# Kernel optimization log

Hardware: AMD Instinct MI355X
Metric: run time of the kernel (lower is better)

## Reference

```python
import jax, jax.numpy as jnp
import numpy as np

MARGIN = 1.0
N, D = 8192, 128
NUM_CLASSES = 1024


def setup_inputs() -> dict:
    key = jax.random.key(0)
    k1, k2, k3 = jax.random.split(key, 3)
    a = jax.random.normal(k1, (N, D), dtype=jnp.float32)
    b = jax.random.normal(k2, (N, D), dtype=jnp.float32)
    # L2-normalize embeddings (standard for metric learning; keeps exp() stable)
    a = a / jnp.linalg.norm(a, axis=1, keepdims=True)
    b = b / jnp.linalg.norm(b, axis=1, keepdims=True)
    labels = jax.random.randint(k3, (N,), 0, NUM_CLASSES, dtype=jnp.int64 if jax.config.jax_enable_x64 else jnp.int32)
    return {"a": a, "b": b, "labels": labels}


def reference(a, b, labels):
    # S[i, j] = a_i . b_j  -- full pairwise similarity, one GEMM
    S = a @ b.T  # [N, N]
    same = labels[:, None] == labels[None, :]  # [N, N]
    eye = jnp.eye(labels.shape[0], dtype=bool)
    pos_mask = same & ~eye          # ordered positive pairs (i != j, same label)
    neg_mask = ~same                # ordered negative pairs (labels differ)
    # V[i] = sum_k in neg(i) exp(margin + S[i, k])
    V = jnp.sum(jnp.where(neg_mask, jnp.exp(MARGIN + S), 0.0), axis=1)  # [N]
    # per positive pair (i, j): max(log(V_i + V_j) - S_ij, 0)^2
    hinge = jnp.maximum(jnp.log(V[:, None] + V[None, :]) - S, 0.0)
    comp = jnp.where(pos_mask, hinge * hinge, 0.0)
    num_pos = jnp.sum(pos_mask)
    loss = jnp.sum(comp) / (2.0 * num_pos.astype(S.dtype))
    return loss
```

## Files before the change

kernel.cpp:

```cpp
#include <hip/hip_runtime.h>

#define NN 8192
#define DD 128
#define MAXCLS 64
#define NCHUNK 8
#define LOG2E 1.4426950408889634f
#define E1    2.718281828459045f

typedef __attribute__((ext_vector_type(8))) short bf16x8;
typedef __attribute__((ext_vector_type(4))) float f32x4;

#if __has_builtin(__builtin_amdgcn_exp2f)
#define EXP2F(x) __builtin_amdgcn_exp2f(x)
#else
#define EXP2F(x) exp2f(x)
#endif

__device__ __forceinline__ void load16_lds(const unsigned short* g, unsigned short* l) {
    __builtin_amdgcn_global_load_lds(
        (const __attribute__((address_space(1))) unsigned int*)g,
        (__attribute__((address_space(3))) unsigned int*)l,
        16, 0, 0);
}

__device__ __forceinline__ unsigned short f2bf(float x) {
    unsigned u = __float_as_uint(x);
    u = (u + 0x7FFFu + ((u >> 16) & 1u)) >> 16;
    return (unsigned short)u;
}

__global__ __launch_bounds__(256) void ml_convert_kernel(
    const float* __restrict__ a, const float* __restrict__ b,
    const int* __restrict__ labels,
    unsigned short* __restrict__ abf, unsigned short* __restrict__ bbf,
    int* __restrict__ cnt, int* __restrict__ list)
{
    int t = blockIdx.x * 256 + threadIdx.x;
    const float* src = a;
    unsigned short* dst = abf;
    int idx = t;
    float scale = LOG2E;
    if (t >= 262144) { src = b; dst = bbf; idx = t - 262144; scale = 1.0f; }
    float4 v = ((const float4*)src)[idx];
    ushort4 o;
    o.x = f2bf(v.x * scale); o.y = f2bf(v.y * scale);
    o.z = f2bf(v.z * scale); o.w = f2bf(v.w * scale);
    ((ushort4*)dst)[idx] = o;

    if (t < NN) {
        int c = labels[t];
        int p = atomicAdd(&cnt[c], 1);
        if (p < MAXCLS) list[c * MAXCLS + p] = t;
    }
}

__global__ __launch_bounds__(256, 2) void ml_vsum_gemm_kernel(
    const unsigned short* __restrict__ abf, const unsigned short* __restrict__ bbf,
    float* __restrict__ Vp)
{
    __shared__ unsigned short As[128 * DD];
    __shared__ unsigned short Bs[2][64 * DD];
    __shared__ float red[2][64];

    const int tid  = threadIdx.x;
    const int lane = tid & 63;
    const int wv   = tid >> 6;
    const int row0 = blockIdx.y * 128;
    const int j0   = blockIdx.x * 1024;

    const int lr = lane >> 4;
    const int sp = lane & 15;
    const int m  = lane & 15;
    const int q  = lane >> 4;
    const int xr = m & 7;

#pragma unroll
    for (int i = 0; i < 8; i++) {
        int rb = wv * 32 + i * 4;
        int r  = rb + lr;
        int cc = sp ^ (r & 7);
        load16_lds(&abf[(size_t)(row0 + r) * DD + cc * 8], &As[rb * DD]);
    }
#pragma unroll
    for (int i = 0; i < 4; i++) {
        int rb = wv * 16 + i * 4;
        int r  = rb + lr;
        int cc = sp ^ (r & 7);
        load16_lds(&bbf[(size_t)(j0 + r) * DD + cc * 8], &Bs[0][rb * DD]);
    }
#pragma unroll
    for (int i = 0; i < 4; i++) {
        int rb = wv * 16 + i * 4;
        int r  = rb + lr;
        int cc = sp ^ (r & 7);
        load16_lds(&bbf[(size_t)(j0 + 64 + r) * DD + cc * 8], &Bs[1][rb * DD]);
    }
    __syncthreads();

    const int wi = (wv >> 1) * 64;
    const int wj = (wv & 1) * 32;

    bf16x8 afr[4][4];
#pragma unroll
    for (int ti = 0; ti < 4; ti++)
#pragma unroll
        for (int ks = 0; ks < 4; ks++) {
            int r   = wi + ti * 16 + m;
            int pos = (ks * 4 + q) ^ xr;
            afr[ti][ks] = *(const bf16x8*)(&As[r * DD + pos * 8]);
        }

    float rs[4][4];
#pragma unroll
    for (int ti = 0; ti < 4; ti++)
#pragma unroll
        for (int rg = 0; rg < 4; rg++) rs[ti][rg] = 0.f;

    const f32x4 zero = {0.f, 0.f, 0.f, 0.f};

#pragma unroll 2
    for (int jt = 0; jt < 16; jt++) {
        const int pb = jt & 1;
        f32x4 acc[4][2];
#pragma unroll
        for (int ti = 0; ti < 4; ti++)
#pragma unroll
            for (int tj = 0; tj < 2; tj++) acc[ti][tj] = zero;

#pragma unroll
        for (int ks = 0; ks < 4; ks++) {
            bf16x8 bfr[2];
#pragma unroll
            for (int tj = 0; tj < 2; tj++) {
                int r   = wj + tj * 16 + m;
                int pos = (ks * 4 + q) ^ xr;
                bfr[tj] = *(const bf16x8*)(&Bs[pb][r * DD + pos * 8]);
            }
#pragma unroll
            for (int ti = 0; ti < 4; ti++)
#pragma unroll
                for (int tj = 0; tj < 2; tj++)
                    acc[ti][tj] = __builtin_amdgcn_mfma_f32_16x16x32_bf16(afr[ti][ks], bfr[tj], acc[ti][tj], 0, 0, 0);
        }

#pragma unroll
        for (int ti = 0; ti < 4; ti++)
#pragma unroll
            for (int tj = 0; tj < 2; tj++) {
                f32x4 c = acc[ti][tj];
                rs[ti][0] += EXP2F(c[0]);
                rs[ti][1] += EXP2F(c[1]);
                rs[ti][2] += EXP2F(c[2]);
                rs[ti][3] += EXP2F(c[3]);
            }

        __syncthreads();
        if (jt < 14) {
            int jb = j0 + (jt + 2) * 64;
#pragma unroll
            for (int i = 0; i < 4; i++) {
                int rb = wv * 16 + i * 4;
                int r  = rb + lr;
                int cc = sp ^ (r & 7);
                load16_lds(&bbf[(size_t)(jb + r) * DD + cc * 8], &Bs[pb][rb * DD]);
            }
        }
    }

#pragma unroll
    for (int ti = 0; ti < 4; ti++)
#pragma unroll
        for (int rg = 0; rg < 4; rg++) {
            float v = rs[ti][rg];
            v += __shfl_xor(v, 1);
            v += __shfl_xor(v, 2);
            v += __shfl_xor(v, 4);
            v += __shfl_xor(v, 8);
            rs[ti][rg] = v;
        }

    if ((wv & 1) == 1 && m == 0) {
#pragma unroll
        for (int ti = 0; ti < 4; ti++)
#pragma unroll
            for (int rg = 0; rg < 4; rg++)
                red[wv >> 1][ti * 16 + q * 4 + rg] = rs[ti][rg];
    }
    __syncthreads();
    if ((wv & 1) == 0 && m == 0) {
#pragma unroll
        for (int ti = 0; ti < 4; ti++)
#pragma unroll
            for (int rg = 0; rg < 4; rg++) {
                int rloc = ti * 16 + q * 4 + rg;
                Vp[(size_t)blockIdx.x * NN + row0 + wi + rloc] = rs[ti][rg] + red[wv >> 1][rloc];
            }
    }
}

__global__ __launch_bounds__(256) void ml_pairs_kernel(
    const float* __restrict__ a, const float* __restrict__ b,
    const int* __restrict__ cnt, const int* __restrict__ list,
    const float* __restrict__ Vp,
    float* __restrict__ classLoss, int* __restrict__ classCnt)
{
    __shared__ int   mem[MAXCLS];
    __shared__ float sumExp[MAXCLS];
    __shared__ float Vadj[MAXCLS];
    __shared__ float Sc[MAXCLS * MAXCLS];
    __shared__ float ps[4];
    __shared__ int   cs[4];

    const int c   = blockIdx.x;
    const int tid = threadIdx.x;
    int mc = cnt[c];
    if (mc > MAXCLS) mc = MAXCLS;

    float vsum = 0.f;
    if (tid < mc) {
        int r = list[c * MAXCLS + tid];
        mem[tid] = r;
#pragma unroll
        for (int jc = 0; jc < NCHUNK; jc++) vsum += Vp[(size_t)jc * NN + r];
    }
    if (tid < MAXCLS) sumExp[tid] = 0.f;
    __syncthreads();

    const int g = tid >> 4;
    const int l = tid & 15;
    const int tot1 = mc * mc;
    for (int pp = g; pp < tot1; pp += 16) {
        int i = pp / mc;
        int j = pp - i * mc;
        int ri = mem[i], rj = mem[j];
        const float4* ar = (const float4*)(a + (size_t)ri * DD) + l * 2;
        const float4* br = (const float4*)(b + (size_t)rj * DD) + l * 2;
        float4 a0 = ar[0], a1 = ar[1];
        float4 b0 = br[0], b1 = br[1];
        float s = 0.f;
        s = fmaf(a0.x, b0.x, s); s = fmaf(a0.y, b0.y, s);
        s = fmaf(a0.z, b0.z, s); s = fmaf(a0.w, b0.w, s);
        s = fmaf(a1.x, b1.x, s); s = fmaf(a1.y, b1.y, s);
        s = fmaf(a1.z, b1.z, s); s = fmaf(a1.w, b1.w, s);
        s += __shfl_xor(s, 1);
        s += __shfl_xor(s, 2);
        s += __shfl_xor(s, 4);
        s += __shfl_xor(s, 8);
        if (l == 0) {
            Sc[i * MAXCLS + j] = s;
            atomicAdd(&sumExp[i], __expf(s));
        }
    }
    __syncthreads();

    if (tid < mc) Vadj[tid] = E1 * (vsum - sumExp[tid]);
    __syncthreads();

    float partial = 0.f;
    int   count   = 0;
    for (int pp = tid; pp < tot1; pp += 256) {
        int i = pp / mc;
        int j = pp - i * mc;
        if (i != j) {
            float h = fmaxf(logf(Vadj[i] + Vadj[j]) - Sc[i * MAXCLS + j], 0.f);
            partial += h * h;
            count++;
        }
    }
    for (int off = 32; off > 0; off >>= 1) {
        partial += __shfl_down(partial, off);
        count   += __shfl_down(count, off);
    }
    const int lane = tid & 63, wv = tid >> 6;
    if (lane == 0) { ps[wv] = partial; cs[wv] = count; }
    __syncthreads();
    if (tid == 0) {
        classLoss[c] = ps[0] + ps[1] + ps[2] + ps[3];
        classCnt[c]  = cs[0] + cs[1] + cs[2] + cs[3];
    }
}

__global__ __launch_bounds__(256) void ml_finalize_kernel(
    const float* __restrict__ classLoss, const int* __restrict__ classCnt,
    float* __restrict__ out)
{
    __shared__ double dred[4];
    __shared__ long long cred[4];
    const int tid = threadIdx.x;
    const int lane = tid & 63, wv = tid >> 6;

    double dls = 0.0;
    long long dct = 0;
    for (int k = tid; k < 1024; k += 256) {
        dls += (double)classLoss[k];
        dct += (long long)classCnt[k];
    }
    for (int off = 32; off > 0; off >>= 1) {
        dls += __shfl_down(dls, off);
        dct += __shfl_down(dct, off);
    }
    if (lane == 0) { dred[wv] = dls; cred[wv] = dct; }
    __syncthreads();
    if (tid == 0) {
        double ls = dred[0] + dred[1] + dred[2] + dred[3];
        long long np = cred[0] + cred[1] + cred[2] + cred[3];
        out[0] = (float)(ls / (2.0 * (double)np));
    }
}

extern "C" void kernel_launch(void* const* d_in, const int* in_sizes, int n_in,
                              void* d_out, int out_size, void* d_ws, size_t ws_size,
                              hipStream_t stream)
{
    const float* a      = (const float*)d_in[0];
    const float* b      = (const float*)d_in[1];
    const int*   labels = (const int*)d_in[2];
    float* out = (float*)d_out;

    char* ws = (char*)d_ws;
    unsigned short* abf = (unsigned short*)ws;
    unsigned short* bbf = (unsigned short*)(ws + 2097152);
    char*     base2     = ws + 4194304;
    int*      cnt       = (int*)(base2);
    float*    classLoss = (float*)(base2 + 8192);
    int*      classCnt  = (int*)(base2 + 12288);
    int*      list      = (int*)(base2 + 16384);
    float*    Vp        = (float*)(base2 + 278528);

    (void)hipMemsetAsync(cnt, 0, 4096, stream);

    ml_convert_kernel<<<2048, 256, 0, stream>>>(a, b, labels, abf, bbf, cnt, list);

    dim3 g(NCHUNK, NN / 128);
    ml_vsum_gemm_kernel<<<g, 256, 0, stream>>>(abf, bbf, Vp);

    ml_pairs_kernel<<<1024, 256, 0, stream>>>(a, b, cnt, list, Vp, classLoss, classCnt);

    ml_finalize_kernel<<<1, 256, 0, stream>>>(classLoss, classCnt, out);
}
```

Measured before the change: 104.7 us.

## Split GEMM column range finer, drop A LDS staging, bin labels in pairs kernel

The V-sum GEMM now splits the column range into 16 chunks instead of 8, doubling the grid. Each wave owns 32 rows by 64 columns, with its A fragments loaded straight from global memory instead of staged through LDS. The cross-wave LDS reduction is removed, and launch bounds are raised to allow 4 blocks per CU. Label binning moves out of the convert kernel: each class block scans all labels itself, which removes the memset and the global atomics. The costs are more partial V sums for the pairs kernel to combine and a redundant label scan in every class block.

New measurement: 118.1 us. 1.13x slower.

```diff
diff --git a/kernel.cpp b/kernel.cpp
--- a/kernel.cpp
+++ b/kernel.cpp
@@ -3,7 +3,7 @@
 #define NN 8192
 #define DD 128
 #define MAXCLS 64
-#define NCHUNK 8
+#define NCHUNK 16
 #define LOG2E 1.4426950408889634f
 #define E1    2.718281828459045f
 
@@ -31,9 +31,7 @@
 
 __global__ __launch_bounds__(256) void ml_convert_kernel(
     const float* __restrict__ a, const float* __restrict__ b,
-    const int* __restrict__ labels,
-    unsigned short* __restrict__ abf, unsigned short* __restrict__ bbf,
-    int* __restrict__ cnt, int* __restrict__ list)
+    unsigned short* __restrict__ abf, unsigned short* __restrict__ bbf)
 {
     int t = blockIdx.x * 256 + threadIdx.x;
     const float* src = a;
@@ -46,27 +44,18 @@
     o.x = f2bf(v.x * scale); o.y = f2bf(v.y * scale);
     o.z = f2bf(v.z * scale); o.w = f2bf(v.w * scale);
     ((ushort4*)dst)[idx] = o;
-
-    if (t < NN) {
-        int c = labels[t];
-        int p = atomicAdd(&cnt[c], 1);
-        if (p < MAXCLS) list[c * MAXCLS + p] = t;
-    }
-}
-
-__global__ __launch_bounds__(256, 2) void ml_vsum_gemm_kernel(
+}
+
+__global__ __launch_bounds__(256, 4) void ml_vsum_gemm_kernel(
     const unsigned short* __restrict__ abf, const unsigned short* __restrict__ bbf,
     float* __restrict__ Vp)
 {
-    __shared__ unsigned short As[128 * DD];
     __shared__ unsigned short Bs[2][64 * DD];
-    __shared__ float red[2][64];
-
     const int tid  = threadIdx.x;
     const int lane = tid & 63;
     const int wv   = tid >> 6;
     const int row0 = blockIdx.y * 128;
-    const int j0   = blockIdx.x * 1024;
+    const int j0   = blockIdx.x * 512;
 
     const int lr = lane >> 4;
     const int sp = lane & 15;
@@ -75,13 +64,6 @@
     const int xr = m & 7;
 
 #pragma unroll
-    for (int i = 0; i < 8; i++) {
-        int rb = wv * 32 + i * 4;
-        int r  = rb + lr;
-        int cc = sp ^ (r & 7);
-        load16_lds(&abf[(size_t)(row0 + r) * DD + cc * 8], &As[rb * DD]);
-    }
-#pragma unroll
     for (int i = 0; i < 4; i++) {
         int rb = wv * 16 + i * 4;
         int r  = rb + lr;
@@ -95,58 +77,53 @@
         int cc = sp ^ (r & 7);
         load16_lds(&bbf[(size_t)(j0 + 64 + r) * DD + cc * 8], &Bs[1][rb * DD]);
     }
-    __syncthreads();
-
-    const int wi = (wv >> 1) * 64;
-    const int wj = (wv & 1) * 32;
-
-    bf16x8 afr[4][4];
-#pragma unroll
-    for (int ti = 0; ti < 4; ti++)
+
+    const int wi = wv * 32;
+    bf16x8 afr[2][4];
+#pragma unroll
+    for (int ti = 0; ti < 2; ti++)
+#pragma unroll
+        for (int ks = 0; ks < 4; ks++)
+            afr[ti][ks] = *(const bf16x8*)(&abf[(size_t)(row0 + wi + ti * 16 + m) * DD + (ks * 4 + q) * 8]);
+
+    float rs[2][4];
+#pragma unroll
+    for (int ti = 0; ti < 2; ti++)
+#pragma unroll
+        for (int rg = 0; rg < 4; rg++) rs[ti][rg] = 0.f;
+
+    const f32x4 zero = {0.f, 0.f, 0.f, 0.f};
+    __syncthreads();
+
+#pragma unroll 2
+    for (int jt = 0; jt < 8; jt++) {
+        const int pb = jt & 1;
+        f32x4 acc[2][4];
+#pragma unroll
+        for (int ti = 0; ti < 2; ti++)
+#pragma unroll
+            for (int tj = 0; tj < 4; tj++) acc[ti][tj] = zero;
+
 #pragma unroll
         for (int ks = 0; ks < 4; ks++) {
-            int r   = wi + ti * 16 + m;
-            int pos = (ks * 4 + q) ^ xr;
-            afr[ti][ks] = *(const bf16x8*)(&As[r * DD + pos * 8]);
-        }
-
-    float rs[4][4];
-#pragma unroll
-    for (int ti = 0; ti < 4; ti++)
-#pragma unroll
-        for (int rg = 0; rg < 4; rg++) rs[ti][rg] = 0.f;
-
-    const f32x4 zero = {0.f, 0.f, 0.f, 0.f};
-
-#pragma unroll 2
-    for (int jt = 0; jt < 16; jt++) {
-        const int pb = jt & 1;
-        f32x4 acc[4][2];
-#pragma unroll
-        for (int ti = 0; ti < 4; ti++)
-#pragma unroll
-            for (int tj = 0; tj < 2; tj++) acc[ti][tj] = zero;
-
-#pragma unroll
-        for (int ks = 0; ks < 4; ks++) {
-            bf16x8 bfr[2];
-#pragma unroll
-            for (int tj = 0; tj < 2; tj++) {
-                int r   = wj + tj * 16 + m;
+            bf16x8 bfr[4];
+#pragma unroll
+            for (int tj = 0; tj < 4; tj++) {
+                int r   = tj * 16 + m;
                 int pos = (ks * 4 + q) ^ xr;
                 bfr[tj] = *(const bf16x8*)(&Bs[pb][r * DD + pos * 8]);
             }
 #pragma unroll
-            for (int ti = 0; ti < 4; ti++)
-#pragma unroll
-                for (int tj = 0; tj < 2; tj++)
+            for (int ti = 0; ti < 2; ti++)
+#pragma unroll
+                for (int tj = 0; tj < 4; tj++)
                     acc[ti][tj] = __builtin_amdgcn_mfma_f32_16x16x32_bf16(afr[ti][ks], bfr[tj], acc[ti][tj], 0, 0, 0);
         }
 
 #pragma unroll
-        for (int ti = 0; ti < 4; ti++)
-#pragma unroll
-            for (int tj = 0; tj < 2; tj++) {
+        for (int ti = 0; ti < 2; ti++)
+#pragma unroll
+            for (int tj = 0; tj < 4; tj++) {
                 f32x4 c = acc[ti][tj];
                 rs[ti][0] += EXP2F(c[0]);
                 rs[ti][1] += EXP2F(c[1]);
@@ -155,7 +132,7 @@
             }
 
         __syncthreads();
-        if (jt < 14) {
+        if (jt < 6) {
             int jb = j0 + (jt + 2) * 64;
 #pragma unroll
             for (int i = 0; i < 4; i++) {
@@ -168,7 +145,7 @@
     }
 
 #pragma unroll
-    for (int ti = 0; ti < 4; ti++)
+    for (int ti = 0; ti < 2; ti++)
 #pragma unroll
         for (int rg = 0; rg < 4; rg++) {
             float v = rs[ti][rg];
@@ -178,33 +155,22 @@
             v += __shfl_xor(v, 8);
             rs[ti][rg] = v;
         }
-
-    if ((wv & 1) == 1 && m == 0) {
-#pragma unroll
-        for (int ti = 0; ti < 4; ti++)
+    if (m == 0) {
+#pragma unroll
+        for (int ti = 0; ti < 2; ti++)
 #pragma unroll
             for (int rg = 0; rg < 4; rg++)
-                red[wv >> 1][ti * 16 + q * 4 + rg] = rs[ti][rg];
-    }
-    __syncthreads();
-    if ((wv & 1) == 0 && m == 0) {
-#pragma unroll
-        for (int ti = 0; ti < 4; ti++)
-#pragma unroll
-            for (int rg = 0; rg < 4; rg++) {
-                int rloc = ti * 16 + q * 4 + rg;
-                Vp[(size_t)blockIdx.x * NN + row0 + wi + rloc] = rs[ti][rg] + red[wv >> 1][rloc];
-            }
+                Vp[(size_t)blockIdx.x * NN + row0 + wi + ti * 16 + q * 4 + rg] = rs[ti][rg];
     }
 }
 
 __global__ __launch_bounds__(256) void ml_pairs_kernel(
     const float* __restrict__ a, const float* __restrict__ b,
-    const int* __restrict__ cnt, const int* __restrict__ list,
-    const float* __restrict__ Vp,
+    const int* __restrict__ labels, const float* __restrict__ Vp,
     float* __restrict__ classLoss, int* __restrict__ classCnt)
 {
     __shared__ int   mem[MAXCLS];
+    __shared__ int   mcnt;
     __shared__ float sumExp[MAXCLS];
     __shared__ float Vadj[MAXCLS];
     __shared__ float Sc[MAXCLS * MAXCLS];
@@ -213,17 +179,26 @@
 
     const int c   = blockIdx.x;
     const int tid = threadIdx.x;
-    int mc = cnt[c];
+
+    if (tid == 0) mcnt = 0;
+    if (tid < MAXCLS) sumExp[tid] = 0.f;
+    __syncthreads();
+    for (int j = tid; j < NN; j += 256) {
+        if (labels[j] == c) {
+            int p = atomicAdd(&mcnt, 1);
+            if (p < MAXCLS) mem[p] = j;
+        }
+    }
+    __syncthreads();
+    int mc = mcnt;
     if (mc > MAXCLS) mc = MAXCLS;
 
     float vsum = 0.f;
     if (tid < mc) {
-        int r = list[c * MAXCLS + tid];
-        mem[tid] = r;
+        int r = mem[tid];
 #pragma unroll
         for (int jc = 0; jc < NCHUNK; jc++) vsum += Vp[(size_t)jc * NN + r];
     }
-    if (tid < MAXCLS) sumExp[tid] = 0.f;
     __syncthreads();
 
     const int g = tid >> 4;
@@ -320,21 +295,17 @@
     char* ws = (char*)d_ws;
     unsigned short* abf = (unsigned short*)ws;
     unsigned short* bbf = (unsigned short*)(ws + 2097152);
-    char*     base2     = ws + 4194304;
-    int*      cnt       = (int*)(base2);
-    float*    classLoss = (float*)(base2 + 8192);
-    int*      classCnt  = (int*)(base2 + 12288);
-    int*      list      = (int*)(base2 + 16384);
-    float*    Vp        = (float*)(base2 + 278528);
-
-    (void)hipMemsetAsync(cnt, 0, 4096, stream);
-
-    ml_convert_kernel<<<2048, 256, 0, stream>>>(a, b, labels, abf, bbf, cnt, list);
+    char*  base2        = ws + 4194304;
+    float* Vp           = (float*)(base2);
+    float* classLoss    = (float*)(base2 + 524288);
+    int*   classCnt     = (int*)(base2 + 528384);
+
+    ml_convert_kernel<<<2048, 256, 0, stream>>>(a, b, abf, bbf);
 
     dim3 g(NCHUNK, NN / 128);
     ml_vsum_gemm_kernel<<<g, 256, 0, stream>>>(abf, bbf, Vp);
 
-    ml_pairs_kernel<<<1024, 256, 0, stream>>>(a, b, cnt, list, Vp, classLoss, classCnt);
+    ml_pairs_kernel<<<1024, 256, 0, stream>>>(a, b, labels, Vp, classLoss, classCnt);
 
     ml_finalize_kernel<<<1, 256, 0, stream>>>(classLoss, classCnt, out);
 }
```
